# Kernel optimization log

Measured on AMD Instinct MI355X. Metric: run time of the kernel, lower is better.

## Reference

```python
import jax, jax.numpy as jnp
import numpy as np

N_NODES = 20000
N_EDGES = 320000
N_GRAPHS = 512
IN_FEATS = 128
HID = 256
RDKIT_IN = 2048
RDK_H1, RDK_H2 = 1024, 512
COMB_H1, COMB_H2 = 1024, 512
N_TASKS = 1
EPS = 1e-5


def _lin(k, fan_in, fan_out):
    return jax.random.normal(k, (fan_in, fan_out), jnp.float32) / np.float32(np.sqrt(fan_in))


def setup_inputs() -> dict:
    key = jax.random.key(0)
    ks = jax.random.split(key, 24)
    inp = {}
    inp["node_feats"] = jax.random.normal(ks[0], (N_NODES, IN_FEATS), jnp.float32)
    inp["rdkit_feats"] = jax.random.normal(ks[1], (N_GRAPHS, RDKIT_IN), jnp.float32)
    inp["src"] = jax.random.randint(ks[2], (N_EDGES,), 0, N_NODES, dtype=jnp.int32)
    inp["dst"] = jax.random.randint(ks[3], (N_EDGES,), 0, N_NODES, dtype=jnp.int32)
    # sorted graph ids; first N_GRAPHS entries guarantee every graph has >=1 node
    gid = jnp.concatenate([jnp.arange(N_GRAPHS, dtype=jnp.int32),
                           jax.random.randint(ks[4], (N_NODES - N_GRAPHS,), 0, N_GRAPHS, dtype=jnp.int32)])
    inp["node_gid"] = jnp.sort(gid)
    # GCN layer params (GraphConv W,b + residual Linear + BatchNorm gamma/beta)
    dims = [(IN_FEATS, HID), (HID, HID)]
    for i, (fi, fo) in enumerate(dims, start=1):
        inp[f"W{i}"] = _lin(ks[4 + 4 * i], fi, fo)
        inp[f"b{i}"] = jnp.zeros((fo,), jnp.float32)
        inp[f"rW{i}"] = _lin(ks[5 + 4 * i], fi, fo)
        inp[f"rb{i}"] = jnp.zeros((fo,), jnp.float32)
        inp[f"g{i}"] = jnp.ones((fo,), jnp.float32)
        inp[f"be{i}"] = jnp.zeros((fo,), jnp.float32)
    inp["aw_W"] = _lin(ks[16], HID, 1)
    inp["aw_b"] = jnp.zeros((1,), jnp.float32)
    inp["rk_W1"] = _lin(ks[17], RDKIT_IN, RDK_H1)
    inp["rk_b1"] = jnp.zeros((RDK_H1,), jnp.float32)
    inp["rk_W2"] = _lin(ks[18], RDK_H1, RDK_H2)
    inp["rk_b2"] = jnp.zeros((RDK_H2,), jnp.float32)
    comb_in = RDK_H2 + 2 * HID
    inp["c_W1"] = _lin(ks[19], comb_in, COMB_H1)
    inp["c_b1"] = jnp.zeros((COMB_H1,), jnp.float32)
    inp["c_W2"] = _lin(ks[20], COMB_H1, COMB_H2)
    inp["c_b2"] = jnp.zeros((COMB_H2,), jnp.float32)
    inp["c_W3"] = _lin(ks[21], COMB_H2, N_TASKS)
    inp["c_b3"] = jnp.zeros((N_TASKS,), jnp.float32)
    return inp


def _gcn_layer(h, src, dst, W, b, rW, rb, g, be):
    # GraphConv, norm='none': sum incoming messages of (X W), then bias + relu
    m = h @ W                                                    # [N, out]
    agg = jax.ops.segment_sum(m[src], dst, num_segments=h.shape[0])
    new = jax.nn.relu(agg + b)
    # residual Linear with activation (dgllife GCNLayer)
    new = new + jax.nn.relu(h @ rW + rb)
    # BatchNorm1d over nodes (training-mode batch stats; dropout in eval = identity)
    mu = new.mean(axis=0)
    var = new.var(axis=0)
    return g * (new - mu) * jax.lax.rsqrt(var + EPS) + be


def reference(node_feats, rdkit_feats, src, dst, node_gid,
              W1, b1, rW1, rb1, g1, be1,
              W2, b2, rW2, rb2, g2, be2,
              aw_W, aw_b, rk_W1, rk_b1, rk_W2, rk_b2,
              c_W1, c_b1, c_W2, c_b2, c_W3, c_b3):
    h = _gcn_layer(node_feats, src, dst, W1, b1, rW1, rb1, g1, be1)
    h = _gcn_layer(h, src, dst, W2, b2, rW2, rb2, g2, be2)
    # WeightedSumAndMax readout
    w = jax.nn.sigmoid(h @ aw_W + aw_b)                          # [N, 1]
    hg_sum = jax.ops.segment_sum(h * w, node_gid, num_segments=N_GRAPHS)
    hg_max = jax.ops.segment_max(h, node_gid, num_segments=N_GRAPHS)
    graph_feats = jnp.concatenate([hg_sum, hg_max], axis=1)       # [B, 2*HID]
    # RDKit encoder MLP
    r = jax.nn.relu(rdkit_feats @ rk_W1 + rk_b1)
    r = jax.nn.relu(r @ rk_W2 + rk_b2)
    z = jnp.concatenate([graph_feats, r], axis=1)
    z = jax.nn.relu(z @ c_W1 + c_b1)
    z = jax.nn.relu(z @ c_W2 + c_b2)
    return z @ c_W3 + c_b3                                       # [B, n_tasks]
```

## Files before the change

kernel.cpp:

```cpp
#include <hip/hip_runtime.h>
#include <hip/hip_bf16.h>
#include <cstdint>
#include <cstddef>

#define N_NODES 20000
#define N_EDGES 320000
#define N_GRAPHS 512
#define IN_FEATS 128
#define HID 256

typedef __bf16 bhalf;
typedef __bf16 bhalf8 __attribute__((ext_vector_type(8)));
typedef __bf16 bhalf4 __attribute__((ext_vector_type(4)));
typedef __bf16 bhalf2 __attribute__((ext_vector_type(2)));
typedef float f32x4 __attribute__((ext_vector_type(4)));

__device__ __forceinline__ int2 xcd_swz(int bx, int by, int nbx, int nby)
{
    int lid = by * nbx + bx;
    int nwg = nbx * nby;
    int q = nwg >> 3, r = nwg & 7;
    int xcd = lid & 7, loc = lid >> 3;
    int s = (xcd < r ? xcd * (q + 1) : r * (q + 1) + (xcd - r) * q) + loc;
    return make_int2(s % nbx, s / nbx);
}

template<int RELU, int OUTBF16>
__global__ __launch_bounds__(256) void gemm_mfma(const bhalf* __restrict__ A,
                                                 const bhalf* __restrict__ Bt,
                                                 void* __restrict__ Cv,
                                                 const float* __restrict__ bias,
                                                 int M, int K, int ldc)
{
    __shared__ bhalf As[64 * 64];
    __shared__ bhalf Bs[64 * 64];

    const int t = threadIdx.x;
    const int lane = t & 63, wid = t >> 6;
    const int wm0 = (wid >> 1) * 32, wn0 = (wid & 1) * 32;
    int2 bsw = xcd_swz(blockIdx.x, blockIdx.y, gridDim.x, gridDim.y);
    const int m0 = bsw.y * 64, n0 = bsw.x * 64;
    const int S = gridDim.z, kz = blockIdx.z;
    const int Ks = K / S;

    const int srow = t >> 2;
    const int sc0 = (t & 3) << 3;

    f32x4 acc[2][2] = {};
    uint4 ra0, ra1, rb0, rb1;

    const bool mok = (m0 + srow) < M;
    const bhalf* Abase = A + (size_t)(m0 + srow) * K + (size_t)kz * Ks;
    const bhalf* Bbase = Bt + (size_t)(n0 + srow) * K + (size_t)kz * Ks;

    ra0 = mok ? *(const uint4*)(Abase + sc0)      : make_uint4(0u,0u,0u,0u);
    ra1 = mok ? *(const uint4*)(Abase + sc0 + 32) : make_uint4(0u,0u,0u,0u);
    rb0 = *(const uint4*)(Bbase + sc0);
    rb1 = *(const uint4*)(Bbase + sc0 + 32);

    const int swz = (srow & 7) << 3;
    for (int k0 = 0; k0 < Ks; k0 += 64) {
        __syncthreads();
        *(uint4*)&As[srow * 64 + (sc0 ^ swz)]        = ra0;
        *(uint4*)&As[srow * 64 + ((sc0 + 32) ^ swz)] = ra1;
        *(uint4*)&Bs[srow * 64 + (sc0 ^ swz)]        = rb0;
        *(uint4*)&Bs[srow * 64 + ((sc0 + 32) ^ swz)] = rb1;
        __syncthreads();
        if (k0 + 64 < Ks) {
            const bhalf* An = Abase + k0 + 64;
            const bhalf* Bn = Bbase + k0 + 64;
            ra0 = mok ? *(const uint4*)(An + sc0)      : make_uint4(0u,0u,0u,0u);
            ra1 = mok ? *(const uint4*)(An + sc0 + 32) : make_uint4(0u,0u,0u,0u);
            rb0 = *(const uint4*)(Bn + sc0);
            rb1 = *(const uint4*)(Bn + sc0 + 32);
        }
#pragma unroll
        for (int kb = 0; kb < 2; ++kb) {
            const int kc = kb * 32 + (lane >> 4) * 8;
            bhalf8 af[2], bfr[2];
#pragma unroll
            for (int i = 0; i < 2; ++i) {
                int rA = wm0 + i * 16 + (lane & 15);
                af[i] = *(const bhalf8*)&As[rA * 64 + (kc ^ ((rA & 7) << 3))];
                int rB = wn0 + i * 16 + (lane & 15);
                bfr[i] = *(const bhalf8*)&Bs[rB * 64 + (kc ^ ((rB & 7) << 3))];
            }
#pragma unroll
            for (int mi = 0; mi < 2; ++mi)
#pragma unroll
                for (int ni = 0; ni < 2; ++ni)
                    acc[mi][ni] = __builtin_amdgcn_mfma_f32_16x16x32_bf16(
                        af[mi], bfr[ni], acc[mi][ni], 0, 0, 0);
        }
    }

#pragma unroll
    for (int mi = 0; mi < 2; ++mi)
#pragma unroll
        for (int ni = 0; ni < 2; ++ni) {
            int col = n0 + wn0 + ni * 16 + (lane & 15);
            f32x4 v = acc[mi][ni];
            if (S > 1) {
#pragma unroll
                for (int r = 0; r < 4; ++r) {
                    int row = m0 + wm0 + mi * 16 + (lane >> 4) * 4 + r;
                    if (row < M)
                        ((float*)Cv)[((size_t)kz * M + row) * ldc + col] = v[r];
                }
            } else {
                float bb = bias ? bias[col] : 0.f;
#pragma unroll
                for (int r = 0; r < 4; ++r) {
                    int row = m0 + wm0 + mi * 16 + (lane >> 4) * 4 + r;
                    if (row < M) {
                        float x = v[r] + bb;
                        if (RELU) x = fmaxf(x, 0.f);
                        if (OUTBF16) ((bhalf*)Cv)[(size_t)row * ldc + col] = (bhalf)x;
                        else         ((float*)Cv)[(size_t)row * ldc + col] = x;
                    }
                }
            }
        }
}

__global__ __launch_bounds__(256) void gcn_gemm_fused(const bhalf* __restrict__ Aagg,
                                                      const bhalf* __restrict__ Ax,
                                                      const bhalf* __restrict__ BW,
                                                      const bhalf* __restrict__ BrW,
                                                      const float* __restrict__ b,
                                                      const float* __restrict__ rb,
                                                      bhalf* __restrict__ vout,
                                                      float* __restrict__ stats,
                                                      int M, int K)
{
    __shared__ bhalf As[64 * 64];
    __shared__ bhalf Bs[64 * 64];
    __shared__ float ssum[64], ssq[64];

    const int t = threadIdx.x;
    const int lane = t & 63, wid = t >> 6;
    const int wm0 = (wid >> 1) * 32, wn0 = (wid & 1) * 32;
    int2 bsw = xcd_swz(blockIdx.x, blockIdx.y, gridDim.x, gridDim.y);
    const int m0 = bsw.y * 64, n0 = bsw.x * 64;

    const int srow = t >> 2;
    const int sc0 = (t & 3) << 3;
    const int nk = K >> 6;

    f32x4 accM[2][2] = {};
    f32x4 accR[2][2] = {};
    uint4 ra0, ra1, rb0, rb1;

    const bool mok = (m0 + srow) < M;
    const bhalf* A0r = Aagg + (size_t)(m0 + srow) * K;
    const bhalf* A1r = Ax + (size_t)(m0 + srow) * K;
    const bhalf* B0r = BW + (size_t)(n0 + srow) * K;
    const bhalf* B1r = BrW + (size_t)(n0 + srow) * K;

    ra0 = mok ? *(const uint4*)(A0r + sc0)      : make_uint4(0u,0u,0u,0u);
    ra1 = mok ? *(const uint4*)(A0r + sc0 + 32) : make_uint4(0u,0u,0u,0u);
    rb0 = *(const uint4*)(B0r + sc0);
    rb1 = *(const uint4*)(B0r + sc0 + 32);

    const int swz = (srow & 7) << 3;
    const int total = 2 * nk;
    for (int ii = 0; ii < total; ++ii) {
        __syncthreads();
        *(uint4*)&As[srow * 64 + (sc0 ^ swz)]        = ra0;
        *(uint4*)&As[srow * 64 + ((sc0 + 32) ^ swz)] = ra1;
        *(uint4*)&Bs[srow * 64 + (sc0 ^ swz)]        = rb0;
        *(uint4*)&Bs[srow * 64 + ((sc0 + 32) ^ swz)] = rb1;
        __syncthreads();
        int jj = ii + 1;
        if (jj < total) {
            bool seln = jj >= nk;
            int kk = (seln ? jj - nk : jj) << 6;
            const bhalf* Ab = (seln ? A1r : A0r) + kk;
            const bhalf* Bb = (seln ? B1r : B0r) + kk;
            ra0 = mok ? *(const uint4*)(Ab + sc0)      : make_uint4(0u,0u,0u,0u);
            ra1 = mok ? *(const uint4*)(Ab + sc0 + 32) : make_uint4(0u,0u,0u,0u);
            rb0 = *(const uint4*)(Bb + sc0);
            rb1 = *(const uint4*)(Bb + sc0 + 32);
        }
        const bool selc = ii >= nk;
#pragma unroll
        for (int kb = 0; kb < 2; ++kb) {
            const int kc = kb * 32 + (lane >> 4) * 8;
            bhalf8 af[2], bfr[2];
#pragma unroll
            for (int i = 0; i < 2; ++i) {
                int rA = wm0 + i * 16 + (lane & 15);
                af[i] = *(const bhalf8*)&As[rA * 64 + (kc ^ ((rA & 7) << 3))];
                int rB = wn0 + i * 16 + (lane & 15);
                bfr[i] = *(const bhalf8*)&Bs[rB * 64 + (kc ^ ((rB & 7) << 3))];
            }
            if (!selc) {
#pragma unroll
                for (int mi = 0; mi < 2; ++mi)
#pragma unroll
                    for (int ni = 0; ni < 2; ++ni)
                        accM[mi][ni] = __builtin_amdgcn_mfma_f32_16x16x32_bf16(
                            af[mi], bfr[ni], accM[mi][ni], 0, 0, 0);
            } else {
#pragma unroll
                for (int mi = 0; mi < 2; ++mi)
#pragma unroll
                    for (int ni = 0; ni < 2; ++ni)
                        accR[mi][ni] = __builtin_amdgcn_mfma_f32_16x16x32_bf16(
                            af[mi], bfr[ni], accR[mi][ni], 0, 0, 0);
            }
        }
    }

    if (t < 64) { ssum[t] = 0.f; ssq[t] = 0.f; }
    __syncthreads();
    float sloc[2] = {0.f, 0.f}, s2loc[2] = {0.f, 0.f};
#pragma unroll
    for (int ni = 0; ni < 2; ++ni) {
        int cl = wn0 + ni * 16 + (lane & 15);
        int c = n0 + cl;
        float bb = b[c], rbb = rb[c];
#pragma unroll
        for (int mi = 0; mi < 2; ++mi) {
            f32x4 a0v = accM[mi][ni], a1v = accR[mi][ni];
#pragma unroll
            for (int r = 0; r < 4; ++r) {
                int row = m0 + wm0 + mi * 16 + (lane >> 4) * 4 + r;
                if (row < M) {
                    float x = fmaxf(a0v[r] + bb, 0.f) + fmaxf(a1v[r] + rbb, 0.f);
                    vout[(size_t)row * HID + c] = (bhalf)x;
                    sloc[ni] += x;
                    s2loc[ni] += x * x;
                }
            }
        }
        atomicAdd(&ssum[cl], sloc[ni]);
        atomicAdd(&ssq[cl], s2loc[ni]);
    }
    __syncthreads();
    if (t < 64) {
        atomicAdd(&stats[n0 + t], ssum[t]);
        atomicAdd(&stats[HID + n0 + t], ssq[t]);
    }
}

template<int RELU, int OUTBF16>
__global__ __launch_bounds__(256) void splitk_combine(const float* __restrict__ part,
                                                      int S, int M, int N, int ldo,
                                                      const float* __restrict__ bias,
                                                      void* __restrict__ outv)
{
    int i = blockIdx.x * blockDim.x + threadIdx.x;
    int n4 = N >> 2;
    if (i >= M * n4) return;
    int row = i / n4, c4 = (i - row * n4) << 2;
    float4 s = make_float4(0.f, 0.f, 0.f, 0.f);
    for (int z = 0; z < S; ++z) {
        float4 p = *(const float4*)(part + ((size_t)z * M + row) * N + c4);
        s.x += p.x; s.y += p.y; s.z += p.z; s.w += p.w;
    }
    float4 bb = *(const float4*)(bias + c4);
    s.x += bb.x; s.y += bb.y; s.z += bb.z; s.w += bb.w;
    if (RELU) {
        s.x = fmaxf(s.x, 0.f); s.y = fmaxf(s.y, 0.f);
        s.z = fmaxf(s.z, 0.f); s.w = fmaxf(s.w, 0.f);
    }
    if (OUTBF16) {
        bhalf4 o = {(bhalf)s.x, (bhalf)s.y, (bhalf)s.z, (bhalf)s.w};
        *(bhalf4*)((bhalf*)outv + (size_t)row * ldo + c4) = o;
    } else {
        *(float4*)((float*)outv + (size_t)row * ldo + c4) = s;
    }
}

__global__ __launch_bounds__(128) void splitk_combine_dot(const float* __restrict__ part,
                                                          int S, int M, int N,
                                                          const float* __restrict__ bias,
                                                          const float* __restrict__ W3,
                                                          const float* __restrict__ b3,
                                                          float* __restrict__ out)
{
    int row = blockIdx.x, t = threadIdx.x;
    int c4 = t << 2;
    float4 s = make_float4(0.f, 0.f, 0.f, 0.f);
    for (int z = 0; z < S; ++z) {
        float4 p = *(const float4*)(part + ((size_t)z * M + row) * N + c4);
        s.x += p.x; s.y += p.y; s.z += p.z; s.w += p.w;
    }
    float4 bb = *(const float4*)(bias + c4);
    float4 w = *(const float4*)(W3 + c4);
    float d = fmaxf(s.x + bb.x, 0.f) * w.x + fmaxf(s.y + bb.y, 0.f) * w.y
            + fmaxf(s.z + bb.z, 0.f) * w.z + fmaxf(s.w + bb.w, 0.f) * w.w;
#pragma unroll
    for (int off = 32; off > 0; off >>= 1) d += __shfl_xor(d, off);
    __shared__ float ws2[2];
    if ((t & 63) == 0) ws2[t >> 6] = d;
    __syncthreads();
    if (t == 0) out[row] = ws2[0] + ws2[1] + b3[0];
}

struct WEnt { const float* src; bhalf* dst; int K; int N; int tiles_end; };
struct PrepTab {
    WEnt e[8];
    const float* ca; bhalf* coa; int n4a;
    const float* cb; bhalf* cob; int n4b;
    uint4* zbase; int zn;
};

#define WTILES 4288
#define CONVB  3524

__global__ __launch_bounds__(256) void prep_batch(PrepTab tab)
{
    __shared__ float tile[32][33];
    int tb = blockIdx.x;
    int t = threadIdx.x;
    if (tb < WTILES) {
        int idx = 0;
#pragma unroll
        for (int i = 0; i < 8; ++i)
            if (tb >= tab.e[i].tiles_end) idx = i + 1;
        const WEnt& E = tab.e[idx];
        int t0 = idx ? tab.e[idx - 1].tiles_end : 0;
        int lt = tb - t0;
        int tX = E.N >> 5;
        int bx = (lt % tX) << 5;
        int by = (lt / tX) << 5;
        int tx = t & 31, ty = t >> 5;
#pragma unroll
        for (int i = 0; i < 32; i += 8)
            tile[ty + i][tx] = E.src[(size_t)(by + ty + i) * E.N + bx + tx];
        __syncthreads();
#pragma unroll
        for (int i = 0; i < 32; i += 8)
            E.dst[(size_t)(bx + ty + i) * E.K + by + tx] = (bhalf)tile[tx][ty + i];
    } else if (tb < WTILES + CONVB) {
        int i = (tb - WTILES) * 256 + t;
        const float* s; bhalf* d; int j;
        if (i < tab.n4a) { s = tab.ca; d = tab.coa; j = i; }
        else { j = i - tab.n4a; if (j >= tab.n4b) return; s = tab.cb; d = tab.cob; }
        float4 v = ((const float4*)s)[j];
        bhalf4 o = {(bhalf)v.x, (bhalf)v.y, (bhalf)v.z, (bhalf)v.w};
        ((bhalf4*)d)[j] = o;
    } else {
        int j = (tb - WTILES - CONVB) * 256 + t;
        if (j < tab.zn) tab.zbase[j] = make_uint4(0u, 0u, 0u, 0u);
    }
}

__global__ void csr_count(const int* __restrict__ dst, int* __restrict__ counts)
{
    int e = blockIdx.x * blockDim.x + threadIdx.x;
    if (e >= N_EDGES) return;
    atomicAdd(&counts[dst[e]], 1);
}

__global__ __launch_bounds__(256) void csr_scan_a(const int* __restrict__ counts,
                                                  int* __restrict__ bsum)
{
    int i = blockIdx.x * 256 + threadIdx.x;
    int v = (i < N_NODES) ? counts[i] : 0;
#pragma unroll
    for (int off = 32; off > 0; off >>= 1) v += __shfl_down(v, off);
    __shared__ int ws[4];
    if ((threadIdx.x & 63) == 0) ws[threadIdx.x >> 6] = v;
    __syncthreads();
    if (threadIdx.x == 0) bsum[blockIdx.x] = ws[0] + ws[1] + ws[2] + ws[3];
}

__global__ __launch_bounds__(256) void csr_scan_c(const int* __restrict__ counts,
                                                  const int* __restrict__ bsum, int nb,
                                                  int* __restrict__ offsets)
{
    int t = threadIdx.x, b = blockIdx.x;
    int i = b * 256 + t;
    int v = (i < N_NODES) ? counts[i] : 0;
    int x = v;
#pragma unroll
    for (int off = 1; off < 64; off <<= 1) {
        int y = __shfl_up(x, off);
        if ((t & 63) >= off) x += y;
    }
    __shared__ int wsum[4];
    __shared__ int tmp[128];
    __shared__ int addsh;
    if ((t & 63) == 63) wsum[t >> 6] = x;
    if (t < 128) tmp[t] = (t < nb) ? bsum[t] : 0;
    __syncthreads();
    if (t == 0) {
        int a = 0;
        for (int j = 0; j < b; ++j) a += tmp[j];
        addsh = a;
    }
    __syncthreads();
    int add = addsh;
    for (int w = 0; w < (t >> 6); ++w) add += wsum[w];
    int excl = x - v + add;
    if (i < N_NODES) offsets[i] = excl;
    if (i == N_NODES - 1) offsets[N_NODES] = excl + v;
}

__global__ void csr_fill(const int* __restrict__ src, const int* __restrict__ dst,
                         const int* __restrict__ offsets, int* __restrict__ cursor,
                         int* __restrict__ eidx)
{
    int e = blockIdx.x * blockDim.x + threadIdx.x;
    if (e >= N_EDGES) return;
    int d = dst[e];
    int slot = offsets[d] + atomicAdd(&cursor[d], 1);
    eidx[slot] = src[e];
}

__global__ void csr_sort_wave(const int* __restrict__ offsets, int* __restrict__ eidx)
{
    int gidx = blockIdx.x * blockDim.x + threadIdx.x;
    int n = gidx >> 6, lane = gidx & 63;
    if (n >= N_NODES) return;
    int lo = offsets[n], hi = offsets[n + 1];
    int cnt = hi - lo;
    if (cnt <= 1) return;
    if (cnt <= 64) {
        int v = (lane < cnt) ? eidx[lo + lane] : 0x7fffffff;
        int rank = 0;
        for (int j = 0; j < cnt; ++j) {
            int vj = __shfl(v, j);
            if (vj < v || (vj == v && j < lane)) ++rank;
        }
        if (lane < cnt) eidx[lo + rank] = v;
    } else if (lane == 0) {
        for (int i = lo + 1; i < hi; ++i) {
            int v = eidx[i]; int j = i - 1;
            while (j >= lo && eidx[j] > v) { eidx[j + 1] = eidx[j]; --j; }
            eidx[j + 1] = v;
        }
    }
}

__global__ __launch_bounds__(256) void edge_gather1(const bhalf* __restrict__ m,
                                                    const int* __restrict__ offsets,
                                                    const int* __restrict__ eidx,
                                                    bhalf* __restrict__ agg)
{
    int gidx = blockIdx.x * blockDim.x + threadIdx.x;
    int n = gidx >> 6, lane = gidx & 63;
    if (n >= N_NODES) return;
    int lo = offsets[n], hi = offsets[n + 1];
    int sub = lane >> 4;
    int colb = (lane & 15) * 8;
    float acc[8] = {};
    int i = lo;
    for (; i + 8 <= hi; i += 8) {
        bhalf8 v0 = *(const bhalf8*)(m + (size_t)eidx[i + sub] * IN_FEATS + colb);
        bhalf8 v1 = *(const bhalf8*)(m + (size_t)eidx[i + 4 + sub] * IN_FEATS + colb);
#pragma unroll
        for (int j = 0; j < 8; ++j) acc[j] += (float)v0[j] + (float)v1[j];
    }
    if (i + 4 <= hi) {
        bhalf8 v0 = *(const bhalf8*)(m + (size_t)eidx[i + sub] * IN_FEATS + colb);
#pragma unroll
        for (int j = 0; j < 8; ++j) acc[j] += (float)v0[j];
        i += 4;
    }
    if (i < hi && sub < hi - i) {
        bhalf8 v0 = *(const bhalf8*)(m + (size_t)eidx[i + sub] * IN_FEATS + colb);
#pragma unroll
        for (int j = 0; j < 8; ++j) acc[j] += (float)v0[j];
    }
#pragma unroll
    for (int j = 0; j < 8; ++j) {
        acc[j] += __shfl_xor(acc[j], 16);
        acc[j] += __shfl_xor(acc[j], 32);
    }
    if (sub == 0) {
        bhalf8 o;
#pragma unroll
        for (int j = 0; j < 8; ++j) o[j] = (bhalf)acc[j];
        *(bhalf8*)(agg + (size_t)n * IN_FEATS + colb) = o;
    }
}

__global__ __launch_bounds__(256) void edge_gather2(const bhalf* __restrict__ m,
                                                    const int* __restrict__ offsets,
                                                    const int* __restrict__ eidx,
                                                    bhalf* __restrict__ agg)
{
    int gidx = blockIdx.x * blockDim.x + threadIdx.x;
    int n = gidx >> 6, lane = gidx & 63;
    if (n >= N_NODES) return;
    int lo = offsets[n], hi = offsets[n + 1];
    int sub = lane >> 5;
    int colb = (lane & 31) * 8;
    float acc[8] = {};
    int i = lo;
    for (; i + 8 <= hi; i += 8) {
        bhalf8 v0 = *(const bhalf8*)(m + (size_t)eidx[i + sub] * HID + colb);
        bhalf8 v1 = *(const bhalf8*)(m + (size_t)eidx[i + 2 + sub] * HID + colb);
        bhalf8 v2 = *(const bhalf8*)(m + (size_t)eidx[i + 4 + sub] * HID + colb);
        bhalf8 v3 = *(const bhalf8*)(m + (size_t)eidx[i + 6 + sub] * HID + colb);
#pragma unroll
        for (int j = 0; j < 8; ++j)
            acc[j] += ((float)v0[j] + (float)v1[j]) + ((float)v2[j] + (float)v3[j]);
    }
    for (; i + 2 <= hi; i += 2) {
        bhalf8 v0 = *(const bhalf8*)(m + (size_t)eidx[i + sub] * HID + colb);
#pragma unroll
        for (int j = 0; j < 8; ++j) acc[j] += (float)v0[j];
    }
    if (i < hi && sub == 0) {
        bhalf8 v0 = *(const bhalf8*)(m + (size_t)eidx[i] * HID + colb);
#pragma unroll
        for (int j = 0; j < 8; ++j) acc[j] += (float)v0[j];
    }
#pragma unroll
    for (int j = 0; j < 8; ++j)
        acc[j] += __shfl_xor(acc[j], 32);
    if (sub == 0) {
        bhalf8 o;
#pragma unroll
        for (int j = 0; j < 8; ++j) o[j] = (bhalf)acc[j];
        *(bhalf8*)(agg + (size_t)n * HID + colb) = o;
    }
}

template<int MODE>
__global__ __launch_bounds__(256) void bn_row(const bhalf* __restrict__ v,
                                              const float* __restrict__ stats,
                                              float inv_n,
                                              const float* __restrict__ g,
                                              const float* __restrict__ be,
                                              bhalf* __restrict__ outb,
                                              const float* __restrict__ awW,
                                              const float* __restrict__ awb,
                                              float* __restrict__ w)
{
    int gidx = blockIdx.x * blockDim.x + threadIdx.x;
    int n = gidx >> 6, lane = gidx & 63;
    if (n >= N_NODES) return;
    int col = lane * 4;
    bhalf4 vv = *(const bhalf4*)(v + (size_t)n * HID + col);
    float4 sm = *(const float4*)(stats + col);
    float4 sq = *(const float4*)(stats + HID + col);
    float4 gg = *(const float4*)(g + col);
    float4 bb = *(const float4*)(be + col);
    float mux = sm.x * inv_n, muy = sm.y * inv_n, muz = sm.z * inv_n, muw = sm.w * inv_n;
    float rsx = rsqrtf(sq.x * inv_n - mux * mux + 1e-5f);
    float rsy = rsqrtf(sq.y * inv_n - muy * muy + 1e-5f);
    float rsz = rsqrtf(sq.z * inv_n - muz * muz + 1e-5f);
    float rsw = rsqrtf(sq.w * inv_n - muw * muw + 1e-5f);
    float4 o;
    o.x = gg.x * ((float)vv.x - mux) * rsx + bb.x;
    o.y = gg.y * ((float)vv.y - muy) * rsy + bb.y;
    o.z = gg.z * ((float)vv.z - muz) * rsz + bb.z;
    o.w = gg.w * ((float)vv.w - muw) * rsw + bb.w;
    bhalf4 ob = {(bhalf)o.x, (bhalf)o.y, (bhalf)o.z, (bhalf)o.w};
    *(bhalf4*)(outb + (size_t)n * HID + col) = ob;
    if (MODE == 1) {
        float4 wv = *(const float4*)(awW + col);
        float d = o.x * wv.x + o.y * wv.y + o.z * wv.z + o.w * wv.w;
#pragma unroll
        for (int off = 32; off > 0; off >>= 1) d += __shfl_xor(d, off);
        if (lane == 0) w[n] = 1.f / (1.f + expf(-(d + awb[0])));
    }
}

__global__ __launch_bounds__(256) void readout(const bhalf* __restrict__ h,
                                               const float* __restrict__ w,
                                               const int* __restrict__ gid,
                                               bhalf* __restrict__ z)
{
    int g = blockIdx.x, col = threadIdx.x;
    int lo = 0, hi = N_NODES;
    while (lo < hi) { int mid = (lo + hi) >> 1; if (gid[mid] < g) lo = mid + 1; else hi = mid; }
    int start = lo;
    hi = N_NODES;
    while (lo < hi) { int mid = (lo + hi) >> 1; if (gid[mid] <= g) lo = mid + 1; else hi = mid; }
    int end = lo;
    float s = 0.f, mx = -INFINITY;
    for (int n = start; n < end; ++n) {
        float v = (float)h[(size_t)n * HID + col];
        s = fmaf(v, w[n], s);
        mx = fmaxf(mx, v);
    }
    z[(size_t)g * 1024 + col] = (bhalf)s;
    z[(size_t)g * 1024 + HID + col] = (bhalf)mx;
}

extern "C" void kernel_launch(void* const* d_in, const int* in_sizes, int n_in,
                              void* d_out, int out_size, void* d_ws, size_t ws_size,
                              hipStream_t stream)
{
    (void)in_sizes; (void)n_in; (void)out_size; (void)ws_size;

    const float* node_feats = (const float*)d_in[0];
    const float* rdkit      = (const float*)d_in[1];
    const int*   src        = (const int*)d_in[2];
    const int*   dst        = (const int*)d_in[3];
    const int*   gid        = (const int*)d_in[4];
    const float* W1  = (const float*)d_in[5];
    const float* b1  = (const float*)d_in[6];
    const float* rW1 = (const float*)d_in[7];
    const float* rb1 = (const float*)d_in[8];
    const float* g1  = (const float*)d_in[9];
    const float* be1 = (const float*)d_in[10];
    const float* W2  = (const float*)d_in[11];
    const float* b2  = (const float*)d_in[12];
    const float* rW2 = (const float*)d_in[13];
    const float* rb2 = (const float*)d_in[14];
    const float* g2  = (const float*)d_in[15];
    const float* be2 = (const float*)d_in[16];
    const float* aw_W  = (const float*)d_in[17];
    const float* aw_b  = (const float*)d_in[18];
    const float* rk_W1 = (const float*)d_in[19];
    const float* rk_b1 = (const float*)d_in[20];
    const float* rk_W2 = (const float*)d_in[21];
    const float* rk_b2 = (const float*)d_in[22];
    const float* c_W1  = (const float*)d_in[23];
    const float* c_b1  = (const float*)d_in[24];
    const float* c_W2  = (const float*)d_in[25];
    const float* c_b2  = (const float*)d_in[26];
    const float* c_W3  = (const float*)d_in[27];
    const float* c_b3  = (const float*)d_in[28];

    float* out = (float*)d_out;

    const size_t NODE = (size_t)N_NODES * HID;
    bhalf* nfb   = (bhalf*)d_ws;
    bhalf* h1b   = nfb + (size_t)N_NODES * IN_FEATS;
    bhalf* h2b   = h1b + NODE;
    bhalf* aggb  = h2b + NODE;
    bhalf* vb    = aggb + NODE;
    bhalf* W1cat = vb + NODE;
    bhalf* W2cat = W1cat + 512 * 128;
    bhalf* rkW1t = W2cat + 512 * 256;
    bhalf* rkW2t = rkW1t + 2048 * 1024;
    bhalf* cW1t  = rkW2t + 1024 * 512;
    bhalf* cW2t  = cW1t + 1024 * 1024;
    bhalf* rdkb  = cW2t + 1024 * 512;
    float* stats1 = (float*)(rdkb + 512 * 2048);
    float* stats2 = stats1 + 512;
    int*   counts = (int*)(stats2 + 512);
    int*   cursor = counts + N_NODES;
    float* wbuf   = (float*)(cursor + N_NODES);
    int*   offsets = (int*)(wbuf + N_NODES);
    int*   eidx    = offsets + N_NODES + 1;
    int*   bsum    = eidx + N_EDGES;
    bhalf* rkhb  = (bhalf*)(bsum + 128);
    bhalf* zb    = rkhb + 512 * 1024;
    bhalf* ch1b  = zb + 512 * 1024;
    float* spart = (float*)(ch1b + 512 * 1024);

    dim3 blk(256);
    const int EPB = (N_EDGES + 255) / 256;
    const int NPB = (N_NODES + 255) / 256;
    const int NWAVE = (N_NODES * 64) / 256;
    dim3 gfused(HID / 64, (N_NODES + 63) / 64);

    PrepTab tab;
    tab.e[0] = {W1,    W1cat,             128, 256,   32};
    tab.e[1] = {rW1,   W1cat + 256 * 128, 128, 256,   64};
    tab.e[2] = {W2,    W2cat,             256, 256,  128};
    tab.e[3] = {rW2,   W2cat + 256 * 256, 256, 256,  192};
    tab.e[4] = {rk_W1, rkW1t,            2048, 1024, 2240};
    tab.e[5] = {rk_W2, rkW2t,            1024, 512,  2752};
    tab.e[6] = {c_W1,  cW1t,             1024, 1024, 3776};
    tab.e[7] = {c_W2,  cW2t,             1024, 512,  4288};
    tab.ca = node_feats; tab.coa = nfb;  tab.n4a = N_NODES * IN_FEATS / 4;
    tab.cb = rdkit;      tab.cob = rdkb; tab.n4b = 512 * 2048 / 4;
    tab.zbase = (uint4*)stats1;
    tab.zn = (1024 + 2 * N_NODES) / 4;
    const int ZB = (tab.zn + 255) / 256;
    prep_batch<<<WTILES + CONVB + ZB, blk, 0, stream>>>(tab);

    csr_count<<<EPB, blk, 0, stream>>>(dst, counts);
    csr_scan_a<<<NPB, blk, 0, stream>>>(counts, bsum);
    csr_scan_c<<<NPB, blk, 0, stream>>>(counts, bsum, NPB, offsets);
    csr_fill<<<EPB, blk, 0, stream>>>(src, dst, offsets, cursor, eidx);
    csr_sort_wave<<<NWAVE, blk, 0, stream>>>(offsets, eidx);

    edge_gather1<<<NWAVE, blk, 0, stream>>>(nfb, offsets, eidx, aggb);
    gcn_gemm_fused<<<gfused, blk, 0, stream>>>(aggb, nfb, W1cat, W1cat + 256 * 128,
                                               b1, rb1, vb, stats1, N_NODES, IN_FEATS);
    bn_row<0><<<NWAVE, blk, 0, stream>>>(vb, stats1, 1.0f / N_NODES, g1, be1,
                                         h1b, nullptr, nullptr, nullptr);

    edge_gather2<<<NWAVE, blk, 0, stream>>>(h1b, offsets, eidx, aggb);
    gcn_gemm_fused<<<gfused, blk, 0, stream>>>(aggb, h1b, W2cat, W2cat + 256 * 256,
                                               b2, rb2, vb, stats2, N_NODES, HID);
    bn_row<1><<<NWAVE, blk, 0, stream>>>(vb, stats2, 1.0f / N_NODES, g2, be2,
                                         h2b, aw_W, aw_b, wbuf);

    readout<<<N_GRAPHS, HID, 0, stream>>>(h2b, wbuf, gid, zb);

    gemm_mfma<0,0><<<dim3(16, 8, 8), blk, 0, stream>>>(rdkb, rkW1t, spart, nullptr,
                                                       512, 2048, 1024);
    splitk_combine<1,1><<<512, blk, 0, stream>>>(spart, 8, 512, 1024, 1024, rk_b1, rkhb);
    gemm_mfma<0,0><<<dim3(8, 8, 8), blk, 0, stream>>>(rkhb, rkW2t, spart, nullptr,
                                                      512, 1024, 512);
    splitk_combine<1,1><<<256, blk, 0, stream>>>(spart, 8, 512, 512, 1024, rk_b2, zb + 512);

    gemm_mfma<0,0><<<dim3(16, 8, 4), blk, 0, stream>>>(zb, cW1t, spart, nullptr,
                                                       512, 1024, 1024);
    splitk_combine<1,1><<<512, blk, 0, stream>>>(spart, 4, 512, 1024, 1024, c_b1, ch1b);
    gemm_mfma<0,0><<<dim3(8, 8, 8), blk, 0, stream>>>(ch1b, cW2t, spart, nullptr,
                                                      512, 1024, 512);
    splitk_combine_dot<<<512, 128, 0, stream>>>(spart, 8, 512, 512, c_b2, c_W3, c_b3, out);
}
```

Baseline: 233.0 us.

## Fold first-layer BatchNorm into edge gather and second GCN GEMM

```diff
diff --git a/kernel.cpp b/kernel.cpp
--- a/kernel.cpp
+++ b/kernel.cpp
@@ -123,6 +123,7 @@
         }
 }
 
+template<int BN>
 __global__ __launch_bounds__(256) void gcn_gemm_fused(const bhalf* __restrict__ Aagg,
                                                       const bhalf* __restrict__ Ax,
                                                       const bhalf* __restrict__ BW,
@@ -131,11 +132,16 @@
                                                       const float* __restrict__ rb,
                                                       bhalf* __restrict__ vout,
                                                       float* __restrict__ stats,
-                                                      int M, int K)
+                                                      int M, int K,
+                                                      const float* __restrict__ bnstats,
+                                                      const float* __restrict__ bng,
+                                                      const float* __restrict__ bnbe,
+                                                      float inv_n)
 {
     __shared__ bhalf As[64 * 64];
     __shared__ bhalf Bs[64 * 64];
     __shared__ float ssum[64], ssq[64];
+    __shared__ float bnS[256], bnB[256];
 
     const int t = threadIdx.x;
     const int lane = t & 63, wid = t >> 6;
@@ -147,6 +153,14 @@
     const int sc0 = (t & 3) << 3;
     const int nk = K >> 6;
 
+    if (BN && t < K) {
+        float mu = bnstats[t] * inv_n;
+        float rs = rsqrtf(bnstats[K + t] * inv_n - mu * mu + 1e-5f);
+        float s = bng[t] * rs;
+        bnS[t] = s;
+        bnB[t] = bnbe[t] - mu * s;
+    }
+
     f32x4 accM[2][2] = {};
     f32x4 accR[2][2] = {};
     uint4 ra0, ra1, rb0, rb1;
@@ -164,8 +178,19 @@
 
     const int swz = (srow & 7) << 3;
     const int total = 2 * nk;
+    if (BN) __syncthreads();
     for (int ii = 0; ii < total; ++ii) {
         __syncthreads();
+        if (BN && ii >= nk) {
+            int kb0 = ((ii - nk) << 6) + sc0;
+            bhalf8 a0 = *(bhalf8*)&ra0, a1 = *(bhalf8*)&ra1;
+#pragma unroll
+            for (int j = 0; j < 8; ++j) {
+                a0[j] = (bhalf)((float)a0[j] * bnS[kb0 + j] + bnB[kb0 + j]);
+                a1[j] = (bhalf)((float)a1[j] * bnS[kb0 + 32 + j] + bnB[kb0 + 32 + j]);
+            }
+            ra0 = *(uint4*)&a0; ra1 = *(uint4*)&a1;
+        }
         *(uint4*)&As[srow * 64 + (sc0 ^ swz)]        = ra0;
         *(uint4*)&As[srow * 64 + ((sc0 + 32) ^ swz)] = ra1;
         *(uint4*)&Bs[srow * 64 + (sc0 ^ swz)]        = rb0;
@@ -479,10 +504,14 @@
     }
 }
 
-__global__ __launch_bounds__(256) void edge_gather2(const bhalf* __restrict__ m,
-                                                    const int* __restrict__ offsets,
-                                                    const int* __restrict__ eidx,
-                                                    bhalf* __restrict__ agg)
+__global__ __launch_bounds__(256) void edge_gather2_bn(const bhalf* __restrict__ m,
+                                                       const int* __restrict__ offsets,
+                                                       const int* __restrict__ eidx,
+                                                       const float* __restrict__ bnstats,
+                                                       const float* __restrict__ bng,
+                                                       const float* __restrict__ bnbe,
+                                                       float inv_n,
+                                                       bhalf* __restrict__ agg)
 {
     int gidx = blockIdx.x * blockDim.x + threadIdx.x;
     int n = gidx >> 6, lane = gidx & 63;
@@ -515,23 +544,30 @@
     for (int j = 0; j < 8; ++j)
         acc[j] += __shfl_xor(acc[j], 32);
     if (sub == 0) {
+        float d = (float)(hi - lo);
         bhalf8 o;
 #pragma unroll
-        for (int j = 0; j < 8; ++j) o[j] = (bhalf)acc[j];
+        for (int j = 0; j < 8; ++j) {
+            int c = colb + j;
+            float mu = bnstats[c] * inv_n;
+            float rs = rsqrtf(bnstats[HID + c] * inv_n - mu * mu + 1e-5f);
+            float s = bng[c] * rs;
+            float tt = bnbe[c] - mu * s;
+            o[j] = (bhalf)(acc[j] * s + d * tt);
+        }
         *(bhalf8*)(agg + (size_t)n * HID + colb) = o;
     }
 }
 
-template<int MODE>
-__global__ __launch_bounds__(256) void bn_row(const bhalf* __restrict__ v,
-                                              const float* __restrict__ stats,
-                                              float inv_n,
-                                              const float* __restrict__ g,
-                                              const float* __restrict__ be,
-                                              bhalf* __restrict__ outb,
-                                              const float* __restrict__ awW,
-                                              const float* __restrict__ awb,
-                                              float* __restrict__ w)
+__global__ __launch_bounds__(256) void bn_row_aw(const bhalf* __restrict__ v,
+                                                 const float* __restrict__ stats,
+                                                 float inv_n,
+                                                 const float* __restrict__ g,
+                                                 const float* __restrict__ be,
+                                                 bhalf* __restrict__ outb,
+                                                 const float* __restrict__ awW,
+                                                 const float* __restrict__ awb,
+                                                 float* __restrict__ w)
 {
     int gidx = blockIdx.x * blockDim.x + threadIdx.x;
     int n = gidx >> 6, lane = gidx & 63;
@@ -554,13 +590,11 @@
     o.w = gg.w * ((float)vv.w - muw) * rsw + bb.w;
     bhalf4 ob = {(bhalf)o.x, (bhalf)o.y, (bhalf)o.z, (bhalf)o.w};
     *(bhalf4*)(outb + (size_t)n * HID + col) = ob;
-    if (MODE == 1) {
-        float4 wv = *(const float4*)(awW + col);
-        float d = o.x * wv.x + o.y * wv.y + o.z * wv.z + o.w * wv.w;
-#pragma unroll
-        for (int off = 32; off > 0; off >>= 1) d += __shfl_xor(d, off);
-        if (lane == 0) w[n] = 1.f / (1.f + expf(-(d + awb[0])));
-    }
+    float4 wv = *(const float4*)(awW + col);
+    float d = o.x * wv.x + o.y * wv.y + o.z * wv.z + o.w * wv.w;
+#pragma unroll
+    for (int off = 32; off > 0; off >>= 1) d += __shfl_xor(d, off);
+    if (lane == 0) w[n] = 1.f / (1.f + expf(-(d + awb[0])));
 }
 
 __global__ __launch_bounds__(256) void readout(const bhalf* __restrict__ h,
@@ -625,11 +659,11 @@
 
     const size_t NODE = (size_t)N_NODES * HID;
     bhalf* nfb   = (bhalf*)d_ws;
-    bhalf* h1b   = nfb + (size_t)N_NODES * IN_FEATS;
-    bhalf* h2b   = h1b + NODE;
+    bhalf* h2b   = nfb + (size_t)N_NODES * IN_FEATS;
     bhalf* aggb  = h2b + NODE;
     bhalf* vb    = aggb + NODE;
-    bhalf* W1cat = vb + NODE;
+    bhalf* vb2   = vb + NODE;
+    bhalf* W1cat = vb2 + NODE;
     bhalf* W2cat = W1cat + 512 * 128;
     bhalf* rkW1t = W2cat + 512 * 256;
     bhalf* rkW2t = rkW1t + 2048 * 1024;
@@ -678,22 +712,23 @@
     csr_sort_wave<<<NWAVE, blk, 0, stream>>>(offsets, eidx);
 
     edge_gather1<<<NWAVE, blk, 0, stream>>>(nfb, offsets, eidx, aggb);
-    gcn_gemm_fused<<<gfused, blk, 0, stream>>>(aggb, nfb, W1cat, W1cat + 256 * 128,
-                                               b1, rb1, vb, stats1, N_NODES, IN_FEATS);
-    bn_row<0><<<NWAVE, blk, 0, stream>>>(vb, stats1, 1.0f / N_NODES, g1, be1,
-                                         h1b, nullptr, nullptr, nullptr);
-
-    edge_gather2<<<NWAVE, blk, 0, stream>>>(h1b, offsets, eidx, aggb);
-    gcn_gemm_fused<<<gfused, blk, 0, stream>>>(aggb, h1b, W2cat, W2cat + 256 * 256,
-                                               b2, rb2, vb, stats2, N_NODES, HID);
-    bn_row<1><<<NWAVE, blk, 0, stream>>>(vb, stats2, 1.0f / N_NODES, g2, be2,
+    gcn_gemm_fused<0><<<gfused, blk, 0, stream>>>(aggb, nfb, W1cat, W1cat + 256 * 128,
+                                                  b1, rb1, vb, stats1, N_NODES, IN_FEATS,
+                                                  nullptr, nullptr, nullptr, 0.f);
+
+    edge_gather2_bn<<<NWAVE, blk, 0, stream>>>(vb, offsets, eidx,
+                                               stats1, g1, be1, 1.0f / N_NODES, aggb);
+    gcn_gemm_fused<1><<<gfused, blk, 0, stream>>>(aggb, vb, W2cat, W2cat + 256 * 256,
+                                                  b2, rb2, vb2, stats2, N_NODES, HID,
+                                                  stats1, g1, be1, 1.0f / N_NODES);
+    bn_row_aw<<<NWAVE, blk, 0, stream>>>(vb2, stats2, 1.0f / N_NODES, g2, be2,
                                          h2b, aw_W, aw_b, wbuf);
 
     readout<<<N_GRAPHS, HID, 0, stream>>>(h2b, wbuf, gid, zb);
 
-    gemm_mfma<0,0><<<dim3(16, 8, 8), blk, 0, stream>>>(rdkb, rkW1t, spart, nullptr,
+    gemm_mfma<0,0><<<dim3(16, 8, 4), blk, 0, stream>>>(rdkb, rkW1t, spart, nullptr,
                                                        512, 2048, 1024);
-    splitk_combine<1,1><<<512, blk, 0, stream>>>(spart, 8, 512, 1024, 1024, rk_b1, rkhb);
+    splitk_combine<1,1><<<512, blk, 0, stream>>>(spart, 4, 512, 1024, 1024, rk_b1, rkhb);
     gemm_mfma<0,0><<<dim3(8, 8, 8), blk, 0, stream>>>(rkhb, rkW2t, spart, nullptr,
                                                       512, 1024, 512);
     splitk_combine<1,1><<<256, blk, 0, stream>>>(spart, 8, 512, 512, 1024, rk_b2, zb + 512);
```

Result: no change. 230.2 us (-1.2%).
